# Performance work log

Measured on AMD Instinct MI355X. Metric: run time of the kernel, lower is better.

## Reference

```python
import jax, jax.numpy as jnp
import numpy as np

N_NODES = 100000


def setup_inputs() -> dict:
    key = jax.random.key(0)
    k1, k2, k3, k4, k5 = jax.random.split(key, 5)
    n_edges = 3200000
    in_f, out_f = 256, 256
    X = jax.random.normal(k1, (N_NODES, in_f), dtype=jnp.float32)
    edge_src = jax.random.randint(k2, (n_edges,), 0, N_NODES, dtype=jnp.int32)
    edge_dst = jax.random.randint(k3, (n_edges,), 0, N_NODES, dtype=jnp.int32)
    edge_val = jax.random.uniform(k4, (n_edges,), dtype=jnp.float32)
    # kaiming-uniform-like init for weight (out_f, in_f)
    bound = np.sqrt(6.0 / in_f)
    W = jax.random.uniform(k5, (out_f, in_f), dtype=jnp.float32, minval=-bound, maxval=bound)
    b = jnp.zeros((out_f,), dtype=jnp.float32)
    return {"X": X, "edge_src": edge_src, "edge_dst": edge_dst,
            "edge_val": edge_val, "W": W, "b": b}


def reference(X, edge_src, edge_dst, edge_val, W, b):
    # S = A @ X, where A is COO sparse: A[src, dst] = val
    # gather neighbor features, scale by edge value, scatter-add to src rows
    msgs = edge_val[:, None] * X[edge_dst]              # [E, in_f]
    S = jax.ops.segment_sum(msgs, edge_src, num_segments=N_NODES)  # [N, in_f]
    # dense projection + bias: (A X) W^T + b
    return S @ W.T + b
```

## Files before the change

### kernel.cpp

```cpp
#include <hip/hip_runtime.h>

#define NNODES 100000
#define F 256
#define NBKT ((NNODES + 127) / 128)
#define BKT_CAP 5120
#define CHUNK_A 24576

typedef unsigned short u16;
typedef unsigned int   u32;
typedef __attribute__((ext_vector_type(8))) short short8v;
typedef __attribute__((ext_vector_type(8))) unsigned short ushort8;
typedef __attribute__((ext_vector_type(4))) float f32x4;
typedef __attribute__((ext_vector_type(2))) float f32x2;

__device__ __forceinline__ u16 f2bf(float f) {
    u32 u = __float_as_uint(f);
    u32 r = u + 0x7FFFu + ((u >> 16) & 1u);
    return (u16)(r >> 16);
}

__global__ __launch_bounds__(256) void cast_w_init(const float* __restrict__ W,
                                                   u16* __restrict__ Wb,
                                                   int* __restrict__ cur) {
    int i = blockIdx.x * 256 + threadIdx.x;
    if (i < F * F / 4) {
        float4 w = ((const float4*)W)[i];
        ushort4 o;
        o.x = f2bf(w.x); o.y = f2bf(w.y); o.z = f2bf(w.z); o.w = f2bf(w.w);
        ((ushort4*)Wb)[i] = o;
    }
    if (blockIdx.x == 0) {
        for (int j = threadIdx.x; j < NBKT; j += 256) cur[j] = j * BKT_CAP;
    }
}

__global__ __launch_bounds__(256) void gemm_mfma(const float* __restrict__ X,
                                                 const u16* __restrict__ Wb,
                                                 u16* __restrict__ Yb) {
    const int wave = threadIdx.x >> 6;
    const int lane = threadIdx.x & 63;
    const int lm   = lane & 15;
    const int kg   = lane >> 4;
    const int m0   = blockIdx.x * 128 + wave * 32;
    const int n0   = blockIdx.y * 128;

    f32x4 acc[2][8];
#pragma unroll
    for (int t = 0; t < 2; ++t)
#pragma unroll
        for (int u = 0; u < 8; ++u) acc[t][u] = (f32x4){0.f, 0.f, 0.f, 0.f};

    int rowA[2];
#pragma unroll
    for (int t = 0; t < 2; ++t) {
        int row = m0 + t * 16 + lm;
        rowA[t] = (row < NNODES) ? row : NNODES - 1;
    }

    for (int k0 = 0; k0 < F; k0 += 32) {
        const int kb = k0 + kg * 8;
        short8v aF[2];
#pragma unroll
        for (int t = 0; t < 2; ++t) {
            const float* xr = X + (size_t)rowA[t] * F + kb;
            float4 x0 = *(const float4*)xr;
            float4 x1 = *(const float4*)(xr + 4);
            short8v a;
            a[0] = (short)f2bf(x0.x); a[1] = (short)f2bf(x0.y);
            a[2] = (short)f2bf(x0.z); a[3] = (short)f2bf(x0.w);
            a[4] = (short)f2bf(x1.x); a[5] = (short)f2bf(x1.y);
            a[6] = (short)f2bf(x1.z); a[7] = (short)f2bf(x1.w);
            aF[t] = a;
        }
        short8v bF[8];
#pragma unroll
        for (int u = 0; u < 8; ++u)
            bF[u] = *(const short8v*)(Wb + (size_t)(n0 + u * 16 + lm) * F + kb);
#pragma unroll
        for (int t = 0; t < 2; ++t)
#pragma unroll
            for (int u = 0; u < 8; ++u)
                acc[t][u] = __builtin_amdgcn_mfma_f32_16x16x32_bf16(aF[t], bF[u], acc[t][u], 0, 0, 0);
    }

#pragma unroll
    for (int t = 0; t < 2; ++t) {
        int rbase = m0 + t * 16 + kg * 4;
#pragma unroll
        for (int i = 0; i < 4; ++i) {
            int row = rbase + i;
            if (row < NNODES) {
#pragma unroll
                for (int u = 0; u < 8; ++u)
                    Yb[(size_t)row * F + n0 + u * 16 + lm] = f2bf(acc[t][u][i]);
            }
        }
    }
}

__global__ __launch_bounds__(256) void bin_edges(const int* __restrict__ src,
                                                 const int* __restrict__ dst,
                                                 const float* __restrict__ val,
                                                 int* __restrict__ cur,
                                                 int2* __restrict__ temp,
                                                 int n_edges) {
    __shared__ u32 lpk[CHUNK_A];
    __shared__ int hist[NBKT];
    __shared__ int bas[NBKT];
    const int e0 = blockIdx.x * CHUNK_A;
    for (int i = threadIdx.x; i < NBKT; i += 256) hist[i] = 0;
    __syncthreads();

    for (int k = 0; k < CHUNK_A / 256; ++k) {
        int j = k * 256 + threadIdx.x;
        int e = e0 + j;
        if (e < n_edges) {
            int s = src[e];
            int bkt = s >> 7;
            int l = atomicAdd(&hist[bkt], 1);
            lpk[j] = (u32)l | ((u32)(s & 127) << 15) | ((u32)bkt << 22);
        }
    }
    __syncthreads();
    for (int i = threadIdx.x; i < NBKT; i += 256) {
        int c = hist[i];
        bas[i] = c ? atomicAdd(&cur[i], c) : 0;
    }
    __syncthreads();
    for (int k = 0; k < CHUNK_A / 256; ++k) {
        int j = k * 256 + threadIdx.x;
        int e = e0 + j;
        if (e < n_edges) {
            u32 p   = lpk[j];
            int bkt = (int)(p >> 22);
            int pos = bas[bkt] + (int)(p & 0x7FFFu);
            int sl  = (int)((p >> 15) & 127u);
            temp[pos] = make_int2((sl << 20) | dst[e], __float_as_int(val[e]));
        }
    }
}

__global__ __launch_bounds__(256) void sort_bucket(const int* __restrict__ cur,
                                                   const int2* __restrict__ temp,
                                                   int2* __restrict__ pack,
                                                   int2* __restrict__ nodeseg) {
    __shared__ int2 tl[BKT_CAP];
    __shared__ int h[128];
    __shared__ int curl[128];
    const int b = blockIdx.x;
    const int base = b * BKT_CAP;
    int cnt = cur[b] - base;
    if (cnt > BKT_CAP) cnt = BKT_CAP;
    const int tid = threadIdx.x;

    if (tid < 128) h[tid] = 0;
    __syncthreads();
    for (int j = tid; j < cnt; j += 256) {
        int2 t = temp[base + j];
        tl[j] = t;
        atomicAdd(&h[t.x >> 20], 1);
    }
    __syncthreads();
    for (int off = 1; off < 128; off <<= 1) {
        int x = 0;
        if (tid < 128 && tid >= off) x = h[tid - off];
        __syncthreads();
        if (tid < 128) h[tid] += x;
        __syncthreads();
    }
    if (tid < 128) {
        int incl = h[tid];
        int prev = tid ? h[tid - 1] : 0;
        curl[tid] = base + prev;
        int node = b * 128 + tid;
        if (node < NNODES) nodeseg[node] = make_int2(base + prev, base + incl);
    }
    __syncthreads();
    for (int j = tid; j < cnt; j += 256) {
        int2 p = tl[j];
        int loc = p.x >> 20;
        int pos = atomicAdd(&curl[loc], 1);
        pack[pos] = make_int2((p.x & 0xFFFFF) << 9, p.y);
    }
}

__global__ __launch_bounds__(256) void gather_nodes(const int2* __restrict__ nodeseg,
                                                    const int2* __restrict__ pack,
                                                    const u16* __restrict__ Yb,
                                                    const float* __restrict__ bias,
                                                    float* __restrict__ out) {
    int node = blockIdx.x * 4 + (threadIdx.x >> 6);
    if (node >= NNODES) return;
    const int lane = threadIdx.x & 63;
    const int half = lane >> 5;
    const int l5   = lane & 31;
    const u32 loff = (u32)l5 * 16u;
    const char* Ybc = (const char*)Yb;

    int2 seg = nodeseg[node];
    const int beg = seg.x, end = seg.y;

    f32x2 acc2[4];
#pragma unroll
    for (int i = 0; i < 4; ++i) acc2[i] = (f32x2){0.f, 0.f};

    for (int j = beg; j < end; j += 16) {
        u32 off[8];
        float v[8];
        ushort8 y[8];
#pragma unroll
        for (int q = 0; q < 8; ++q) {
            int idx = j + 2 * q + half;
            int safe = idx < end ? idx : end - 1;
            long long raw = __builtin_nontemporal_load((const long long*)&pack[safe]);
            off[q] = (u32)((unsigned long long)raw & 0xFFFFFFFFull);
            v[q] = (idx < end) ? __int_as_float((int)(raw >> 32)) : 0.f;
        }
#pragma unroll
        for (int q = 0; q < 8; ++q)
            y[q] = *(const ushort8*)(Ybc + (off[q] + loff));
#pragma unroll
        for (int q = 0; q < 8; ++q) {
            f32x2 vv; vv[0] = v[q]; vv[1] = v[q];
            const u32* yp = (const u32*)&y[q];
#pragma unroll
            for (int i = 0; i < 4; ++i) {
                u32 pb = yp[i];
                f32x2 yy;
                yy[0] = __uint_as_float(pb << 16);
                yy[1] = __uint_as_float(pb & 0xFFFF0000u);
                acc2[i] = __builtin_elementwise_fma(yy, vv, acc2[i]);
            }
        }
    }

    float acc[8];
#pragma unroll
    for (int i = 0; i < 4; ++i) { acc[2 * i] = acc2[i][0]; acc[2 * i + 1] = acc2[i][1]; }
#pragma unroll
    for (int i = 0; i < 8; ++i) acc[i] += __shfl_xor(acc[i], 32);

    const int col = l5 * 8 + half * 4;
    float4 bv = *(const float4*)&bias[col];
    f32x4 o;
    o[0] = acc[half * 4 + 0] + bv.x;
    o[1] = acc[half * 4 + 1] + bv.y;
    o[2] = acc[half * 4 + 2] + bv.z;
    o[3] = acc[half * 4 + 3] + bv.w;
    __builtin_nontemporal_store(o, (f32x4*)&out[(size_t)node * F + col]);
}

extern "C" void kernel_launch(void* const* d_in, const int* in_sizes, int n_in,
                              void* d_out, int out_size, void* d_ws, size_t ws_size,
                              hipStream_t stream) {
    const float* X        = (const float*)d_in[0];
    const int*   edge_src = (const int*)d_in[1];
    const int*   edge_dst = (const int*)d_in[2];
    const float* edge_val = (const float*)d_in[3];
    const float* W        = (const float*)d_in[4];
    const float* b        = (const float*)d_in[5];
    float*       out      = (float*)d_out;
    const int n_edges     = in_sizes[1];

    char* base = (char*)d_ws;
    const size_t ybBytes   = (size_t)NNODES * F * sizeof(u16);
    const size_t packBytes = (size_t)NBKT * BKT_CAP * sizeof(int2);
    u16*  Yb      = (u16*)base;
    int2* pack    = (int2*)(base + ybBytes);
    int2* temp    = (int2*)(base + ybBytes + packBytes);
    u16*  Wb      = (u16*)(base + ybBytes + 2 * packBytes);
    int2* nodeseg = (int2*)((char*)Wb + (size_t)F * F * sizeof(u16));
    int*  cur     = (int*)(nodeseg + NNODES);

    cast_w_init<<<(F * F / 4 + 255) / 256, 256, 0, stream>>>(W, Wb, cur);

    dim3 ggrid((NNODES + 127) / 128, F / 128);
    gemm_mfma<<<ggrid, 256, 0, stream>>>(X, Wb, Yb);

    bin_edges<<<(n_edges + CHUNK_A - 1) / CHUNK_A, 256, 0, stream>>>(edge_src, edge_dst, edge_val,
                                                                     cur, temp, n_edges);
    sort_bucket<<<NBKT, 256, 0, stream>>>(cur, temp, pack, nodeseg);

    gather_nodes<<<(NNODES + 3) / 4, 256, 0, stream>>>(nodeseg, pack, Yb, b, out);
}
```

Baseline: 609.9 us.

## Replace bucketed two-pass binning with degree count, scan, and atomic CSR fill

Result: slower. 848.6 us (+39.1%).

```diff
diff --git a/kernel.cpp b/kernel.cpp
--- a/kernel.cpp
+++ b/kernel.cpp
@@ -2,9 +2,8 @@
 
 #define NNODES 100000
 #define F 256
-#define NBKT ((NNODES + 127) / 128)
-#define BKT_CAP 5120
-#define CHUNK_A 24576
+#define SCB 1024
+#define NSCB ((NNODES + SCB - 1) / SCB)
 
 typedef unsigned short u16;
 typedef unsigned int   u32;
@@ -19,9 +18,9 @@
     return (u16)(r >> 16);
 }
 
-__global__ __launch_bounds__(256) void cast_w_init(const float* __restrict__ W,
+__global__ __launch_bounds__(256) void cast_w_zero(const float* __restrict__ W,
                                                    u16* __restrict__ Wb,
-                                                   int* __restrict__ cur) {
+                                                   int* __restrict__ deg) {
     int i = blockIdx.x * 256 + threadIdx.x;
     if (i < F * F / 4) {
         float4 w = ((const float4*)W)[i];
@@ -29,9 +28,7 @@
         o.x = f2bf(w.x); o.y = f2bf(w.y); o.z = f2bf(w.z); o.w = f2bf(w.w);
         ((ushort4*)Wb)[i] = o;
     }
-    if (blockIdx.x == 0) {
-        for (int j = threadIdx.x; j < NBKT; j += 256) cur[j] = j * BKT_CAP;
-    }
+    if (i < NNODES) deg[i] = 0;
 }
 
 __global__ __launch_bounds__(256) void gemm_mfma(const float* __restrict__ X,
@@ -98,89 +95,86 @@
     }
 }
 
-__global__ __launch_bounds__(256) void bin_edges(const int* __restrict__ src,
+__global__ __launch_bounds__(256) void count_deg(const int* __restrict__ src,
+                                                 int* __restrict__ deg, int n_edges) {
+    int stride = gridDim.x * 256;
+    for (int e = blockIdx.x * 256 + threadIdx.x; e < n_edges; e += stride)
+        atomicAdd(&deg[src[e]], 1);
+}
+
+__global__ __launch_bounds__(256) void scan_part(const int* __restrict__ deg,
+                                                 int2* __restrict__ nodeseg,
+                                                 int* __restrict__ bsum) {
+    __shared__ int ts[256];
+    const int t = threadIdx.x;
+    const int n0 = blockIdx.x * SCB + t * 4;
+    int d0 = 0, d1 = 0, d2 = 0, d3 = 0;
+    if (n0 + 0 < NNODES) d0 = deg[n0 + 0];
+    if (n0 + 1 < NNODES) d1 = deg[n0 + 1];
+    if (n0 + 2 < NNODES) d2 = deg[n0 + 2];
+    if (n0 + 3 < NNODES) d3 = deg[n0 + 3];
+    int sum = d0 + d1 + d2 + d3;
+    ts[t] = sum;
+    __syncthreads();
+    for (int off = 1; off < 256; off <<= 1) {
+        int x = (t >= off) ? ts[t - off] : 0;
+        __syncthreads();
+        ts[t] += x;
+        __syncthreads();
+    }
+    int p = ts[t] - sum;
+    if (t == 255) bsum[blockIdx.x] = ts[255];
+    if (n0 + 0 < NNODES) nodeseg[n0 + 0] = make_int2(p, d0);
+    p += d0;
+    if (n0 + 1 < NNODES) nodeseg[n0 + 1] = make_int2(p, d1);
+    p += d1;
+    if (n0 + 2 < NNODES) nodeseg[n0 + 2] = make_int2(p, d2);
+    p += d2;
+    if (n0 + 3 < NNODES) nodeseg[n0 + 3] = make_int2(p, d3);
+}
+
+__global__ __launch_bounds__(256) void scan_top(int* __restrict__ bsum) {
+    __shared__ int s[256];
+    const int t = threadIdx.x;
+    int v = (t < NSCB) ? bsum[t] : 0;
+    s[t] = v;
+    __syncthreads();
+    for (int off = 1; off < 256; off <<= 1) {
+        int x = (t >= off) ? s[t - off] : 0;
+        __syncthreads();
+        s[t] += x;
+        __syncthreads();
+    }
+    if (t < NSCB) bsum[t] = s[t] - v;
+}
+
+__global__ __launch_bounds__(256) void scan_add(int2* __restrict__ nodeseg,
+                                                const int* __restrict__ bsum,
+                                                int* __restrict__ cursor) {
+    const int boff = bsum[blockIdx.x];
+    const int n0 = blockIdx.x * SCB + threadIdx.x * 4;
+#pragma unroll
+    for (int i = 0; i < 4; ++i) {
+        int n = n0 + i;
+        if (n < NNODES) {
+            int2 pd = nodeseg[n];
+            int start = pd.x + boff;
+            nodeseg[n] = make_int2(start, start + pd.y);
+            cursor[n] = start;
+        }
+    }
+}
+
+__global__ __launch_bounds__(256) void fill_pack(const int* __restrict__ src,
                                                  const int* __restrict__ dst,
                                                  const float* __restrict__ val,
-                                                 int* __restrict__ cur,
-                                                 int2* __restrict__ temp,
-                                                 int n_edges) {
-    __shared__ u32 lpk[CHUNK_A];
-    __shared__ int hist[NBKT];
-    __shared__ int bas[NBKT];
-    const int e0 = blockIdx.x * CHUNK_A;
-    for (int i = threadIdx.x; i < NBKT; i += 256) hist[i] = 0;
-    __syncthreads();
-
-    for (int k = 0; k < CHUNK_A / 256; ++k) {
-        int j = k * 256 + threadIdx.x;
-        int e = e0 + j;
-        if (e < n_edges) {
-            int s = src[e];
-            int bkt = s >> 7;
-            int l = atomicAdd(&hist[bkt], 1);
-            lpk[j] = (u32)l | ((u32)(s & 127) << 15) | ((u32)bkt << 22);
-        }
-    }
-    __syncthreads();
-    for (int i = threadIdx.x; i < NBKT; i += 256) {
-        int c = hist[i];
-        bas[i] = c ? atomicAdd(&cur[i], c) : 0;
-    }
-    __syncthreads();
-    for (int k = 0; k < CHUNK_A / 256; ++k) {
-        int j = k * 256 + threadIdx.x;
-        int e = e0 + j;
-        if (e < n_edges) {
-            u32 p   = lpk[j];
-            int bkt = (int)(p >> 22);
-            int pos = bas[bkt] + (int)(p & 0x7FFFu);
-            int sl  = (int)((p >> 15) & 127u);
-            temp[pos] = make_int2((sl << 20) | dst[e], __float_as_int(val[e]));
-        }
-    }
-}
-
-__global__ __launch_bounds__(256) void sort_bucket(const int* __restrict__ cur,
-                                                   const int2* __restrict__ temp,
-                                                   int2* __restrict__ pack,
-                                                   int2* __restrict__ nodeseg) {
-    __shared__ int2 tl[BKT_CAP];
-    __shared__ int h[128];
-    __shared__ int curl[128];
-    const int b = blockIdx.x;
-    const int base = b * BKT_CAP;
-    int cnt = cur[b] - base;
-    if (cnt > BKT_CAP) cnt = BKT_CAP;
-    const int tid = threadIdx.x;
-
-    if (tid < 128) h[tid] = 0;
-    __syncthreads();
-    for (int j = tid; j < cnt; j += 256) {
-        int2 t = temp[base + j];
-        tl[j] = t;
-        atomicAdd(&h[t.x >> 20], 1);
-    }
-    __syncthreads();
-    for (int off = 1; off < 128; off <<= 1) {
-        int x = 0;
-        if (tid < 128 && tid >= off) x = h[tid - off];
-        __syncthreads();
-        if (tid < 128) h[tid] += x;
-        __syncthreads();
-    }
-    if (tid < 128) {
-        int incl = h[tid];
-        int prev = tid ? h[tid - 1] : 0;
-        curl[tid] = base + prev;
-        int node = b * 128 + tid;
-        if (node < NNODES) nodeseg[node] = make_int2(base + prev, base + incl);
-    }
-    __syncthreads();
-    for (int j = tid; j < cnt; j += 256) {
-        int2 p = tl[j];
-        int loc = p.x >> 20;
-        int pos = atomicAdd(&curl[loc], 1);
-        pack[pos] = make_int2((p.x & 0xFFFFF) << 9, p.y);
+                                                 int* __restrict__ cursor,
+                                                 int2* __restrict__ pack, int n_edges) {
+    int stride = gridDim.x * 256;
+    for (int e = blockIdx.x * 256 + threadIdx.x; e < n_edges; e += stride) {
+        int s = src[e];
+        int pos = atomicAdd(&cursor[s], 1);
+        pack[pos] = make_int2(dst[e] << 9, __float_as_int(val[e]));
     }
 }
 
@@ -264,22 +258,25 @@
 
     char* base = (char*)d_ws;
     const size_t ybBytes   = (size_t)NNODES * F * sizeof(u16);
-    const size_t packBytes = (size_t)NBKT * BKT_CAP * sizeof(int2);
+    const size_t packBytes = (size_t)n_edges * sizeof(int2);
     u16*  Yb      = (u16*)base;
     int2* pack    = (int2*)(base + ybBytes);
-    int2* temp    = (int2*)(base + ybBytes + packBytes);
-    u16*  Wb      = (u16*)(base + ybBytes + 2 * packBytes);
+    u16*  Wb      = (u16*)(base + ybBytes + packBytes);
     int2* nodeseg = (int2*)((char*)Wb + (size_t)F * F * sizeof(u16));
-    int*  cur     = (int*)(nodeseg + NNODES);
-
-    cast_w_init<<<(F * F / 4 + 255) / 256, 256, 0, stream>>>(W, Wb, cur);
+    int*  deg     = (int*)(nodeseg + NNODES);
+    int*  cursor  = deg + NNODES;
+    int*  bsum    = cursor + NNODES;
+
+    cast_w_zero<<<(NNODES + 255) / 256, 256, 0, stream>>>(W, Wb, deg);
 
     dim3 ggrid((NNODES + 127) / 128, F / 128);
     gemm_mfma<<<ggrid, 256, 0, stream>>>(X, Wb, Yb);
 
-    bin_edges<<<(n_edges + CHUNK_A - 1) / CHUNK_A, 256, 0, stream>>>(edge_src, edge_dst, edge_val,
-                                                                     cur, temp, n_edges);
-    sort_bucket<<<NBKT, 256, 0, stream>>>(cur, temp, pack, nodeseg);
+    count_deg<<<1024, 256, 0, stream>>>(edge_src, deg, n_edges);
+    scan_part<<<NSCB, 256, 0, stream>>>(deg, nodeseg, bsum);
+    scan_top<<<1, 256, 0, stream>>>(bsum);
+    scan_add<<<NSCB, 256, 0, stream>>>(nodeseg, bsum, cursor);
+    fill_pack<<<1024, 256, 0, stream>>>(edge_src, edge_dst, edge_val, cursor, pack, n_edges);
 
     gather_nodes<<<(NNODES + 3) / 4, 256, 0, stream>>>(nodeseg, pack, Yb, b, out);
 }
```
